# Kernel tuning notes

Hardware: AMD Instinct MI355X
Metric: run time of the kernel (lower is better)

Reference implementation:

```python
import jax, jax.numpy as jnp
import numpy as np

NUM_EMBEDDINGS = 1024
EMBEDDING_DIM = 64
COMMITMENT_COST = 0.25


def setup_inputs() -> dict:
    key = jax.random.key(0)
    k_in, k_cb = jax.random.split(key)
    inputs = jax.random.normal(k_in, (32, 4096, EMBEDDING_DIM), dtype=jnp.float32)
    # matches reset_embeddings(): uniform(-1/num_embeddings, 1/num_embeddings)
    bound = 1.0 / NUM_EMBEDDINGS
    codebook = jax.random.uniform(k_cb, (NUM_EMBEDDINGS, EMBEDDING_DIM),
                                  dtype=jnp.float32, minval=-bound, maxval=bound)
    return {"inputs": inputs, "codebook": codebook}


def reference(inputs, codebook):
    input_shape = inputs.shape
    D = codebook.shape[1]
    x = inputs.reshape(-1, D)  # [N, D]
    # Squared euclidean distances; argmin is invariant to the sqrt used by torch.cdist.
    # dist2[n,k] = ||x_n||^2 - 2 x_n . e_k + ||e_k||^2
    dist2 = (jnp.sum(x * x, axis=1, keepdims=True)
             - 2.0 * (x @ codebook.T)
             + jnp.sum(codebook * codebook, axis=1))  # [N, K]
    encoding_indices = jnp.argmin(dist2, axis=1)  # [N]
    quantized = codebook[encoding_indices].reshape(input_shape)
    loss = (jnp.mean((jax.lax.stop_gradient(quantized) - inputs) ** 2)
            + COMMITMENT_COST * jnp.mean((quantized - jax.lax.stop_gradient(inputs)) ** 2))
    # straight-through estimator
    quantized_st = inputs + jax.lax.stop_gradient(quantized - inputs)
    return quantized_st, loss
```

## Files before the change

### kernel.cpp

```cpp
#include <hip/hip_runtime.h>


typedef __attribute__((ext_vector_type(8))) short short8;
typedef __attribute__((ext_vector_type(4))) float f32x4;

#define VQ_D 64
#define MTILE 512
#define CSTRIDE 68

__device__ inline unsigned short f2bf(float f) {
  union { float f; unsigned u; } v; v.f = f;
  unsigned r = v.u + 0x7FFFu + ((v.u >> 16) & 1u);
  return (unsigned short)(r >> 16);
}

__global__ __launch_bounds__(256) void vq_prep(const float* __restrict__ cb,
                                               float* __restrict__ c2b,
                                               unsigned short* __restrict__ cbb,
                                               float* __restrict__ sse,
                                               unsigned* __restrict__ counter, int K) {
  if (blockIdx.x == 0 && threadIdx.x == 0) { *sse = 0.f; *counter = 0u; }
  int w = (int)((blockIdx.x * 256 + threadIdx.x) >> 6);
  int lane = threadIdx.x & 63;
  if (w >= K) return;
  float v = cb[(size_t)w * VQ_D + lane];
  cbb[(size_t)w * VQ_D + lane] = f2bf(v);
  float s = v * v;
#pragma unroll
  for (int off = 32; off; off >>= 1) s += __shfl_down(s, off);
  if (lane == 0) c2b[w] = s + 0.5f;
}

__global__ __launch_bounds__(512) void vq_main(
    const float* __restrict__ x, const float* __restrict__ cb,
    const float* __restrict__ c2b, const unsigned short* __restrict__ cbb,
    float* __restrict__ out, float* __restrict__ sse_out,
    unsigned* __restrict__ counter, int nblocks) {
  __shared__ unsigned short cbs[1024 * CSTRIDE];
  __shared__ float c2s[1024];
  __shared__ int idxs[MTILE];
  __shared__ float redbuf[8];

  const int tid = threadIdx.x;
  const int wave = tid >> 6;
  const int lane = tid & 63;
  const int quad = lane >> 4;
  const int col = lane & 15;
  const long blockRow0 = (long)blockIdx.x * MTILE;
  const int waveRow0 = wave * 64;

#pragma unroll
  for (int r = 0; r < 16; ++r) {
    int id = r * 512 + tid;
    int code = id >> 3;
    int piece = id & 7;
    short8 v = *(const short8*)(cbb + (size_t)code * VQ_D + piece * 8);
    *(short8*)(cbs + code * CSTRIDE + piece * 8) = v;
  }
  c2s[tid] = c2b[tid];
  c2s[tid + 512] = c2b[tid + 512];

  short8 Af[4][2];
#pragma unroll
  for (int mi = 0; mi < 4; ++mi) {
#pragma unroll
    for (int ks = 0; ks < 2; ++ks) {
      long row = blockRow0 + waveRow0 + mi * 16 + col;
      const f32x4* xp = (const f32x4*)(x + row * VQ_D + ks * 32 + quad * 8);
      f32x4 lo = xp[0];
      f32x4 hi = xp[1];
      short8 a;
      a[0] = (short)f2bf(-2.f * lo[0]); a[1] = (short)f2bf(-2.f * lo[1]);
      a[2] = (short)f2bf(-2.f * lo[2]); a[3] = (short)f2bf(-2.f * lo[3]);
      a[4] = (short)f2bf(-2.f * hi[0]); a[5] = (short)f2bf(-2.f * hi[1]);
      a[6] = (short)f2bf(-2.f * hi[2]); a[7] = (short)f2bf(-2.f * hi[3]);
      Af[mi][ks] = a;
    }
  }

  unsigned bk[4][4];
#pragma unroll
  for (int mi = 0; mi < 4; ++mi)
#pragma unroll
    for (int r = 0; r < 4; ++r) bk[mi][r] = 0xFFFFFFFFu;

  __syncthreads();

  const unsigned short* bbase = cbs + (size_t)col * CSTRIDE + quad * 8;
#pragma unroll 4
  for (int t = 0; t < 64; ++t) {
    const unsigned short* bp = bbase + t * 16 * CSTRIDE;
    short8 b0 = *(const short8*)bp;
    short8 b1 = *(const short8*)(bp + 32);
    float cc = c2s[t * 16 + col];

    f32x4 acc[4];
#pragma unroll
    for (int mi = 0; mi < 4; ++mi) {
      f32x4 a = {cc, cc, cc, cc};
      a = __builtin_amdgcn_mfma_f32_16x16x32_bf16(Af[mi][0], b0, a, 0, 0, 0);
      a = __builtin_amdgcn_mfma_f32_16x16x32_bf16(Af[mi][1], b1, a, 0, 0, 0);
      acc[mi] = a;
    }

    const unsigned code = (unsigned)((t << 4) + col);
#pragma unroll
    for (int mi = 0; mi < 4; ++mi)
#pragma unroll
      for (int r = 0; r < 4; ++r)
        bk[mi][r] = min(bk[mi][r], (__float_as_uint(acc[mi][r]) & 0xFFFFFC00u) | code);
  }

#pragma unroll
  for (int off = 1; off < 16; off <<= 1) {
#pragma unroll
    for (int mi = 0; mi < 4; ++mi)
#pragma unroll
      for (int r = 0; r < 4; ++r) {
        unsigned o = (unsigned)__shfl_xor((int)bk[mi][r], off);
        bk[mi][r] = min(bk[mi][r], o);
      }
  }
  if (col == 0) {
#pragma unroll
    for (int mi = 0; mi < 4; ++mi)
#pragma unroll
      for (int r = 0; r < 4; ++r)
        idxs[waveRow0 + mi * 16 + quad * 4 + r] = (int)(bk[mi][r] & 1023u);
  }
  __syncthreads();

  float sse = 0.f;
  const f32x4* cb4 = (const f32x4*)cb;
  const f32x4* x4 = (const f32x4*)x;
  f32x4* out4 = (f32x4*)out;
#pragma unroll
  for (int i = 0; i < 16; ++i) {
    int f = i * 512 + tid;
    int row_l = f >> 4;
    int d4 = f & 15;
    int idx = idxs[row_l];
    f32x4 cv = cb4[(size_t)idx * 16 + d4];
    long gi = (blockRow0 + row_l) * 16 + d4;
    f32x4 xv = x4[gi];
    out4[gi] = cv;
    f32x4 dv = cv - xv;
    sse += dv[0] * dv[0] + dv[1] * dv[1] + dv[2] * dv[2] + dv[3] * dv[3];
  }
#pragma unroll
  for (int off = 32; off; off >>= 1) sse += __shfl_down(sse, off);
  if (lane == 0) redbuf[wave] = sse;
  __syncthreads();

  if (tid == 0) {
    float s = 0.f;
#pragma unroll
    for (int w = 0; w < 8; ++w) s += redbuf[w];
    atomicAdd(sse_out, s);
    __threadfence();
    unsigned old = atomicAdd(counter, 1u);
    if (old == (unsigned)(nblocks - 1)) {
      float tot = atomicAdd(sse_out, 0.f);
      long nelem = (long)nblocks * MTILE * VQ_D;
      out[nelem] = 1.25f * tot / (float)nelem;
    }
  }
}

extern "C" void kernel_launch(void* const* d_in, const int* in_sizes, int n_in,
                              void* d_out, int out_size, void* d_ws, size_t ws_size,
                              hipStream_t stream) {
  const float* x = (const float*)d_in[0];
  const float* cb = (const float*)d_in[1];
  float* out = (float*)d_out;

  const long n_elem = (long)in_sizes[0];
  const int nrows = (int)(n_elem / VQ_D);
  const int K = in_sizes[1] / VQ_D;
  const int nblocks = nrows / MTILE;

  char* ws = (char*)d_ws;
  float* sse = (float*)ws;
  unsigned* counter = (unsigned*)(ws + 64);
  float* c2b = (float*)(ws + 256);
  unsigned short* cbb = (unsigned short*)(ws + 8192);

  vq_prep<<<dim3((K * 64 + 255) / 256), dim3(256), 0, stream>>>(cb, c2b, cbb, sse, counter, K);
  vq_main<<<dim3(nblocks), dim3(512), 0, stream>>>(x, cb, c2b, cbb, out, sse, counter, nblocks);
}
```

Before: 130.9 us.

## Split codebook across blocks with global atomicMin keys and separate gather kernel

The fused kernel is split in two. The argmin kernel gives each block a 256-row tile and one quarter of the codebook, which cuts shared memory per block and raises the number of blocks and likely occupancy. Partial argmin keys are merged through global atomicMin, and a separate gather kernel then writes the quantized rows and the loss. In exchange, x is read twice more from global memory, atomic traffic is added, and there is an extra launch. The keys buffer is hardcoded to 131072 rows and the prep kernel now assumes K=1024.

```diff
diff --git a/kernel.cpp b/kernel.cpp
--- a/kernel.cpp
+++ b/kernel.cpp
@@ -5,7 +5,6 @@
 typedef __attribute__((ext_vector_type(4))) float f32x4;
 
 #define VQ_D 64
-#define MTILE 512
 #define CSTRIDE 68
 
 __device__ inline unsigned short f2bf(float f) {
@@ -17,12 +16,15 @@
 __global__ __launch_bounds__(256) void vq_prep(const float* __restrict__ cb,
                                                float* __restrict__ c2b,
                                                unsigned short* __restrict__ cbb,
+                                               unsigned* __restrict__ keys,
                                                float* __restrict__ sse,
-                                               unsigned* __restrict__ counter, int K) {
-  if (blockIdx.x == 0 && threadIdx.x == 0) { *sse = 0.f; *counter = 0u; }
-  int w = (int)((blockIdx.x * 256 + threadIdx.x) >> 6);
-  int lane = threadIdx.x & 63;
-  if (w >= K) return;
+                                               unsigned* __restrict__ counter) {
+  int g = blockIdx.x * 256 + threadIdx.x;
+  if (g == 0) { *sse = 0.f; *counter = 0u; }
+  keys[g] = 0xFFFFFFFFu;
+  keys[g + 65536] = 0xFFFFFFFFu;
+  int w = g >> 6;
+  int lane = g & 63;
   float v = cb[(size_t)w * VQ_D + lane];
   cbb[(size_t)w * VQ_D + lane] = f2bf(v);
   float s = v * v;
@@ -31,41 +33,39 @@
   if (lane == 0) c2b[w] = s + 0.5f;
 }
 
-__global__ __launch_bounds__(512) void vq_main(
-    const float* __restrict__ x, const float* __restrict__ cb,
-    const float* __restrict__ c2b, const unsigned short* __restrict__ cbb,
-    float* __restrict__ out, float* __restrict__ sse_out,
-    unsigned* __restrict__ counter, int nblocks) {
-  __shared__ unsigned short cbs[1024 * CSTRIDE];
-  __shared__ float c2s[1024];
-  __shared__ int idxs[MTILE];
-  __shared__ float redbuf[8];
+__global__ __launch_bounds__(256) void vq_argmin(
+    const float* __restrict__ x, const float* __restrict__ c2b,
+    const unsigned short* __restrict__ cbb, unsigned* __restrict__ keys) {
+  __shared__ unsigned short cbs[256 * CSTRIDE];
+  __shared__ float c2s[256];
+  __shared__ unsigned keybuf[256];
 
   const int tid = threadIdx.x;
   const int wave = tid >> 6;
   const int lane = tid & 63;
   const int quad = lane >> 4;
   const int col = lane & 15;
-  const long blockRow0 = (long)blockIdx.x * MTILE;
+  const int quarter = blockIdx.x & 3;
+  const long rowTile0 = (long)(blockIdx.x >> 2) * 256;
   const int waveRow0 = wave * 64;
 
+  const unsigned short* src = cbb + (size_t)quarter * 256 * VQ_D;
 #pragma unroll
-  for (int r = 0; r < 16; ++r) {
-    int id = r * 512 + tid;
+  for (int r = 0; r < 8; ++r) {
+    int id = r * 256 + tid;
     int code = id >> 3;
     int piece = id & 7;
-    short8 v = *(const short8*)(cbb + (size_t)code * VQ_D + piece * 8);
+    short8 v = *(const short8*)(src + code * VQ_D + piece * 8);
     *(short8*)(cbs + code * CSTRIDE + piece * 8) = v;
   }
-  c2s[tid] = c2b[tid];
-  c2s[tid + 512] = c2b[tid + 512];
+  c2s[tid] = c2b[quarter * 256 + tid];
 
   short8 Af[4][2];
 #pragma unroll
   for (int mi = 0; mi < 4; ++mi) {
 #pragma unroll
     for (int ks = 0; ks < 2; ++ks) {
-      long row = blockRow0 + waveRow0 + mi * 16 + col;
+      long row = rowTile0 + waveRow0 + mi * 16 + col;
       const f32x4* xp = (const f32x4*)(x + row * VQ_D + ks * 32 + quad * 8);
       f32x4 lo = xp[0];
       f32x4 hi = xp[1];
@@ -87,8 +87,9 @@
   __syncthreads();
 
   const unsigned short* bbase = cbs + (size_t)col * CSTRIDE + quad * 8;
+  const unsigned cbase = (unsigned)(quarter << 8) | (unsigned)col;
 #pragma unroll 4
-  for (int t = 0; t < 64; ++t) {
+  for (int t = 0; t < 16; ++t) {
     const unsigned short* bp = bbase + t * 16 * CSTRIDE;
     short8 b0 = *(const short8*)bp;
     short8 b1 = *(const short8*)(bp + 32);
@@ -103,7 +104,7 @@
       acc[mi] = a;
     }
 
-    const unsigned code = (unsigned)((t << 4) + col);
+    const unsigned code = cbase | (unsigned)(t << 4);
 #pragma unroll
     for (int mi = 0; mi < 4; ++mi)
 #pragma unroll
@@ -126,42 +127,47 @@
     for (int mi = 0; mi < 4; ++mi)
 #pragma unroll
       for (int r = 0; r < 4; ++r)
-        idxs[waveRow0 + mi * 16 + quad * 4 + r] = (int)(bk[mi][r] & 1023u);
+        keybuf[waveRow0 + mi * 16 + quad * 4 + r] = bk[mi][r];
   }
   __syncthreads();
 
-  float sse = 0.f;
+  atomicMin(&keys[rowTile0 + tid], keybuf[tid]);
+}
+
+__global__ __launch_bounds__(256) void vq_gather(
+    const float* __restrict__ x, const float* __restrict__ cb,
+    const unsigned* __restrict__ keys, float* __restrict__ out,
+    float* __restrict__ sse_out, unsigned* __restrict__ counter,
+    long nelem, int nblocks) {
+  __shared__ float redbuf[4];
+  const int tid = threadIdx.x;
   const f32x4* cb4 = (const f32x4*)cb;
   const f32x4* x4 = (const f32x4*)x;
   f32x4* out4 = (f32x4*)out;
+
+  float sse = 0.f;
 #pragma unroll
-  for (int i = 0; i < 16; ++i) {
-    int f = i * 512 + tid;
-    int row_l = f >> 4;
+  for (int i = 0; i < 8; ++i) {
+    int f = blockIdx.x * 2048 + i * 256 + tid;
+    int row = f >> 4;
     int d4 = f & 15;
-    int idx = idxs[row_l];
+    unsigned idx = keys[row] & 1023u;
     f32x4 cv = cb4[(size_t)idx * 16 + d4];
-    long gi = (blockRow0 + row_l) * 16 + d4;
-    f32x4 xv = x4[gi];
-    out4[gi] = cv;
+    f32x4 xv = x4[f];
+    out4[f] = cv;
     f32x4 dv = cv - xv;
     sse += dv[0] * dv[0] + dv[1] * dv[1] + dv[2] * dv[2] + dv[3] * dv[3];
   }
 #pragma unroll
   for (int off = 32; off; off >>= 1) sse += __shfl_down(sse, off);
-  if (lane == 0) redbuf[wave] = sse;
+  if ((tid & 63) == 0) redbuf[tid >> 6] = sse;
   __syncthreads();
-
   if (tid == 0) {
-    float s = 0.f;
-#pragma unroll
-    for (int w = 0; w < 8; ++w) s += redbuf[w];
-    atomicAdd(sse_out, s);
+    atomicAdd(sse_out, redbuf[0] + redbuf[1] + redbuf[2] + redbuf[3]);
     __threadfence();
     unsigned old = atomicAdd(counter, 1u);
     if (old == (unsigned)(nblocks - 1)) {
       float tot = atomicAdd(sse_out, 0.f);
-      long nelem = (long)nblocks * MTILE * VQ_D;
       out[nelem] = 1.25f * tot / (float)nelem;
     }
   }
@@ -176,15 +182,18 @@
 
   const long n_elem = (long)in_sizes[0];
   const int nrows = (int)(n_elem / VQ_D);
-  const int K = in_sizes[1] / VQ_D;
-  const int nblocks = nrows / MTILE;
 
   char* ws = (char*)d_ws;
   float* sse = (float*)ws;
   unsigned* counter = (unsigned*)(ws + 64);
   float* c2b = (float*)(ws + 256);
   unsigned short* cbb = (unsigned short*)(ws + 8192);
+  unsigned* keys = (unsigned*)(ws + 139264);
 
-  vq_prep<<<dim3((K * 64 + 255) / 256), dim3(256), 0, stream>>>(cb, c2b, cbb, sse, counter, K);
-  vq_main<<<dim3(nblocks), dim3(512), 0, stream>>>(x, cb, c2b, cbb, out, sse, counter, nblocks);
+  const int gather_blocks = nrows / 128;
+
+  vq_prep<<<dim3(256), dim3(256), 0, stream>>>(cb, c2b, cbb, keys, sse, counter);
+  vq_argmin<<<dim3((nrows / 256) * 4), dim3(256), 0, stream>>>(x, c2b, cbb, keys);
+  vq_gather<<<dim3(gather_blocks), dim3(256), 0, stream>>>(
+      x, cb, keys, out, sse, counter, n_elem, gather_blocks);
 }
```

After: 164.7 us. +25.8%, slower.
